# Performance work log

Hardware: AMD Instinct MI355X
Metric: run time of the kernel (lower is better)

## Reference

```python
import jax, jax.numpy as jnp
import numpy as np

DIM = 768
NUM_HEADS = 12
HEAD_DIM = DIM // NUM_HEADS
SCALE = HEAD_DIM ** (-0.5)


def setup_inputs() -> dict:
    key = jax.random.key(0)
    ks = jax.random.split(key, 8)
    B, Nq, Nk, Nv = 2, 2048, 2048, 2048
    init = 0.02
    return {
        "xq": jax.random.normal(ks[0], (B, Nq, DIM), dtype=jnp.float32),
        "xk": jax.random.normal(ks[1], (B, Nk, DIM), dtype=jnp.float32),
        "xv": jax.random.normal(ks[2], (B, Nv, DIM), dtype=jnp.float32),
        # torch nn.Linear weights are [out_features, in_features]; qkv_bias=False
        "Wq": jax.random.normal(ks[3], (DIM, DIM), dtype=jnp.float32) * init,
        "Wk": jax.random.normal(ks[4], (DIM, DIM), dtype=jnp.float32) * init,
        "Wv": jax.random.normal(ks[5], (DIM, DIM), dtype=jnp.float32) * init,
        "Wp": jax.random.normal(ks[6], (DIM, DIM), dtype=jnp.float32) * init,
        "bp": jax.random.normal(ks[7], (DIM,), dtype=jnp.float32) * init,
    }


def reference(xq, xk, xv, Wq, Wk, Wv, Wp, bp):
    B, Nq, C = xq.shape
    H, D = NUM_HEADS, HEAD_DIM
    # linear projections (torch Linear: x @ W.T), split heads -> [B, H, N, D]
    q = (xq @ Wq.T).reshape(B, Nq, H, D).transpose(0, 2, 1, 3)
    k = (xk @ Wk.T).reshape(B, xk.shape[1], H, D).transpose(0, 2, 1, 3)
    v = (xv @ Wv.T).reshape(B, xv.shape[1], H, D).transpose(0, 2, 1, 3)
    # attention scores [B, H, Nq, Nk]
    attn = jnp.einsum("bhqd,bhkd->bhqk", q, k) * SCALE
    attn = jax.nn.softmax(attn, axis=-1)
    # weighted values -> merge heads [B, Nq, C]
    out = jnp.einsum("bhqk,bhkd->bhqd", attn, v)
    out = out.transpose(0, 2, 1, 3).reshape(B, Nq, C)
    return out @ Wp.T + bp
```

## Files before the change

kernel.cpp:

```cpp
#include <hip/hip_runtime.h>
#include <hip/hip_bf16.h>


#define NSEQ 2048
#define CDIM 768
#define NH   12
#define HD   64
#define MTOT 4096
#define XEL  (MTOT*CDIM)
#define WEL  (CDIM*CDIM)
#define X8   (XEL/8)
#define W8   (WEL/8)
#define PSTR 72
#define QSCALE 0.18033688011112042f

typedef __attribute__((ext_vector_type(8))) short bf16x8;
typedef __attribute__((ext_vector_type(4))) float floatx4;

static __device__ __forceinline__ unsigned short f2bf(float f) {
  union { float f; unsigned int u; } v; v.f = f;
  return (unsigned short)((v.u + 0x8000u) >> 16);
}
static __device__ __forceinline__ unsigned pk2bf(float a, float b) {
  unsigned ua = __float_as_uint(a) + 0x8000u;
  unsigned ub = __float_as_uint(b) + 0x8000u;
  return __builtin_amdgcn_perm(ub, ua, 0x07060302);
}

static __device__ __forceinline__ void lds16(const void* g, void* l) {
  __builtin_amdgcn_global_load_lds(
      (const __attribute__((address_space(1))) unsigned int*)g,
      (__attribute__((address_space(3))) unsigned int*)l, 16, 0, 0);
}

__global__ __launch_bounds__(256) void cast_all(
    const float* __restrict__ xq, const float* __restrict__ xk,
    const float* __restrict__ xv, const float* __restrict__ wq,
    const float* __restrict__ wk, const float* __restrict__ wv,
    const float* __restrict__ wp,
    unsigned short* __restrict__ Xq, unsigned short* __restrict__ Xk,
    unsigned short* __restrict__ Xv, unsigned short* __restrict__ Wq,
    unsigned short* __restrict__ Wk, unsigned short* __restrict__ Wv,
    unsigned short* __restrict__ Wp) {
  int i = blockIdx.x * 256 + threadIdx.x;
  const float* s; unsigned short* d; int off;
  if (i < 3 * X8) {
    int t = i / X8; off = i - t * X8;
    s = (t == 0) ? xq : (t == 1) ? xk : xv;
    d = (t == 0) ? Xq : (t == 1) ? Xk : Xv;
  } else {
    int j = i - 3 * X8; int t = j / W8; off = j - t * W8;
    s = (t == 0) ? wq : (t == 1) ? wk : (t == 2) ? wv : wp;
    d = (t == 0) ? Wq : (t == 1) ? Wk : (t == 2) ? Wv : Wp;
  }
  const float4* sp = (const float4*)s + (size_t)off * 2;
  float4 a = sp[0], b = sp[1];
  uint4 o;
  o.x = pk2bf(a.x, a.y); o.y = pk2bf(a.z, a.w);
  o.z = pk2bf(b.x, b.y); o.w = pk2bf(b.z, b.w);
  *(uint4*)(d + (size_t)off * 8) = o;
}

__global__ __launch_bounds__(256) void gemm_qkv(
    const unsigned short* __restrict__ Xq, const unsigned short* __restrict__ Xk,
    const unsigned short* __restrict__ Xv, const unsigned short* __restrict__ Wq,
    const unsigned short* __restrict__ Wk, const unsigned short* __restrict__ Wv,
    unsigned short* __restrict__ Qo, unsigned short* __restrict__ Ko,
    unsigned short* __restrict__ Vo) {
  int i0 = blockIdx.x;
  int mg = i0 & 7; int t0 = i0 >> 3;
  int z = t0 % 3; int u = t0 / 3;
  int xn = u & 7, ysub = u >> 3;
  int y = mg * 4 + ysub;
  const unsigned short* A; const unsigned short* B; int am0, bn0, RA;
  if (z == 0)      { A = Xq; B = Wq; am0 = y * 128; bn0 = xn * 96; RA = 128; }
  else if (z == 1) { A = Xk; B = Wk; am0 = y * 128; bn0 = xn * 96; RA = 128; }
  else             { A = Wv; B = Xv; am0 = xn * 96; bn0 = y * 128; RA = 96; }
  __shared__ __align__(16) unsigned short S[224 * 64];
  int tid = threadIdx.x, lane = tid & 63, wave = tid >> 6;
  int quad = lane >> 4, l15 = lane & 15, l7 = l15 & 7;

  const unsigned short* gptr[7]; int ldo[7];
#pragma unroll
  for (int i = 0; i < 7; i++) {
    int idx = i * 256 + tid;
    int row = idx >> 3, c = (idx & 7) ^ (row & 7);
    gptr[i] = (row < RA ? A + (size_t)(am0 + row) * CDIM
                        : B + (size_t)(bn0 + row - RA) * CDIM) + c * 8;
    ldo[i] = idx * 8;
  }
  floatx4 acc[12];
#pragma unroll
  for (int i = 0; i < 12; i++) acc[i] = (floatx4){0.f, 0.f, 0.f, 0.f};

  for (int k0 = 0; k0 < CDIM; k0 += 64) {
#pragma unroll
    for (int i = 0; i < 7; i++) lds16(gptr[i] + k0, &S[ldo[i]]);
    __syncthreads();
    if (z < 2) {
      int wm = (wave >> 1) * 64, wn = (wave & 1) * 48;
#pragma unroll
      for (int ks = 0; ks < 2; ks++) {
        int csw = ((ks * 4 + quad) ^ l7) * 8;
        bf16x8 af[4], bfr[3];
#pragma unroll
        for (int i = 0; i < 4; i++)
          af[i] = *(const bf16x8*)&S[(wm + i * 16 + l15) * 64 + csw];
#pragma unroll
        for (int j = 0; j < 3; j++)
          bfr[j] = *(const bf16x8*)&S[(128 + wn + j * 16 + l15) * 64 + csw];
#pragma unroll
        for (int mi = 0; mi < 4; mi++)
#pragma unroll
          for (int ni = 0; ni < 3; ni++)
            acc[mi * 3 + ni] = __builtin_amdgcn_mfma_f32_16x16x32_bf16(
                af[mi], bfr[ni], acc[mi * 3 + ni], 0, 0, 0);
      }
    } else {
      int wm = (wave & 1) * 48, wn = (wave >> 1) * 64;
#pragma unroll
      for (int ks = 0; ks < 2; ks++) {
        int csw = ((ks * 4 + quad) ^ l7) * 8;
        bf16x8 af[3], bfr[4];
#pragma unroll
        for (int i = 0; i < 3; i++)
          af[i] = *(const bf16x8*)&S[(wm + i * 16 + l15) * 64 + csw];
#pragma unroll
        for (int j = 0; j < 4; j++)
          bfr[j] = *(const bf16x8*)&S[(96 + wn + j * 16 + l15) * 64 + csw];
#pragma unroll
        for (int mi = 0; mi < 3; mi++)
#pragma unroll
          for (int ni = 0; ni < 4; ni++)
            acc[mi * 4 + ni] = __builtin_amdgcn_mfma_f32_16x16x32_bf16(
                af[mi], bfr[ni], acc[mi * 4 + ni], 0, 0, 0);
      }
    }
    __syncthreads();
  }
  if (z < 2) {
    int wm = (wave >> 1) * 64, wn = (wave & 1) * 48;
#pragma unroll
    for (int mi = 0; mi < 4; mi++)
#pragma unroll
      for (int ni = 0; ni < 3; ni++)
#pragma unroll
        for (int r = 0; r < 4; r++) {
          int grow = am0 + wm + mi * 16 + quad * 4 + r;
          int gcol = bn0 + wn + ni * 16 + l15;
          float v = acc[mi * 3 + ni][r];
          int b = grow >> 11, nq = grow & 2047, h = gcol >> 6, dd = gcol & 63;
          if (z == 0)
            Qo[((size_t)(b * NH + h) * NSEQ + nq) * HD + dd] = f2bf(v * QSCALE);
          else
            Ko[((size_t)(b * NH + h) * NSEQ + nq) * HD + dd] = f2bf(v);
        }
  } else {
    int wm = (wave & 1) * 48, wn = (wave >> 1) * 64;
#pragma unroll
    for (int mi = 0; mi < 3; mi++)
#pragma unroll
      for (int ni = 0; ni < 4; ni++)
#pragma unroll
        for (int r = 0; r < 4; r++) {
          int o = am0 + wm + mi * 16 + quad * 4 + r;
          int mgl = bn0 + wn + ni * 16 + l15;
          int b = mgl >> 11, nq = mgl & 2047;
          Vo[((size_t)b * CDIM + o) * NSEQ + nq] = f2bf(acc[mi * 4 + ni][r]);
        }
  }
}

__global__ __launch_bounds__(256, 3) void attn_kernel(
    const unsigned short* __restrict__ Q, const unsigned short* __restrict__ K,
    const unsigned short* __restrict__ Vt, unsigned short* __restrict__ ctx) {
  int i0 = blockIdx.x;
  int xcd = i0 & 7; int t0 = i0 >> 3;
  int bh = xcd * 3 + (t0 >> 5);
  int qt = t0 & 31;
  int tid = threadIdx.x, lane = tid & 63, wave = tid >> 6;
  int half = wave >> 1, qsub = wave & 1;
  int quad = lane >> 4, l15 = lane & 15, l7 = l15 & 7;
  __shared__ __align__(16) unsigned short Ks[2][64 * 64];
  __shared__ __align__(16) unsigned short Vs[2][64 * 64];
  __shared__ __align__(16) unsigned short Ps[4][16 * PSTR];

  const unsigned short* Qg = Q + ((size_t)bh * NSEQ + qt * 64 + qsub * 32) * HD;
  const unsigned short* Kg = K + ((size_t)bh * NSEQ + half * 1024) * HD;
  const unsigned short* Vg = Vt + (size_t)bh * HD * NSEQ + half * 1024;

  bf16x8 qf[2][2];
#pragma unroll
  for (int qi = 0; qi < 2; qi++)
#pragma unroll
    for (int ks = 0; ks < 2; ks++)
      qf[qi][ks] = *(const bf16x8*)(Qg + (qi * 16 + l15) * HD + ks * 32 + quad * 8);

  bf16x8 ones;
#pragma unroll
  for (int i = 0; i < 8; i++) ones[i] = (short)0x3F80;

  int tid2 = tid & 127;
  int kgo[4], vgo[4], ldst[4];
#pragma unroll
  for (int i = 0; i < 4; i++) {
    int idx = i * 128 + tid2;
    int R = idx >> 3, c = (idx & 7) ^ (R & 7);
    kgo[i] = R * HD + c * 8;
    vgo[i] = R * NSEQ + c * 8;
    ldst[i] = idx * 8;
  }
  unsigned short* Ksh = Ks[half];
  unsigned short* Vsh = Vs[half];
  unsigned short* Pw = &Ps[wave][0];

  floatx4 ol[2];
  floatx4 o[2][4];
#pragma unroll
  for (int qi = 0; qi < 2; qi++) {
    ol[qi] = (floatx4){0.f, 0.f, 0.f, 0.f};
#pragma unroll
    for (int dt = 0; dt < 4; dt++) o[qi][dt] = (floatx4){0.f, 0.f, 0.f, 0.f};
  }

  for (int t = 0; t < 16; t++) {
    int k0 = t * 64;
#pragma unroll
    for (int i = 0; i < 4; i++) {
      lds16(Kg + (size_t)k0 * HD + kgo[i], &Ksh[ldst[i]]);
      lds16(Vg + k0 + vgo[i], &Vsh[ldst[i]]);
    }
    __syncthreads();
    bf16x8 kf[4][2], vf[4][2];
#pragma unroll
    for (int nt = 0; nt < 4; nt++)
#pragma unroll
      for (int x = 0; x < 2; x++)
        kf[nt][x] = *(const bf16x8*)&Ksh[(nt * 16 + l15) * 64 + ((x * 4 + quad) ^ l7) * 8];
#pragma unroll
    for (int dt = 0; dt < 4; dt++)
#pragma unroll
      for (int x = 0; x < 2; x++)
        vf[dt][x] = *(const bf16x8*)&Vsh[(dt * 16 + l15) * 64 + ((x * 4 + quad) ^ l7) * 8];
#pragma unroll
    for (int qi = 0; qi < 2; qi++) {
#pragma unroll
      for (int nt = 0; nt < 4; nt++) {
        floatx4 st = (floatx4){0.f, 0.f, 0.f, 0.f};
        st = __builtin_amdgcn_mfma_f32_16x16x32_bf16(kf[nt][0], qf[qi][0], st, 0, 0, 0);
        st = __builtin_amdgcn_mfma_f32_16x16x32_bf16(kf[nt][1], qf[qi][1], st, 0, 0, 0);
        float p0 = __builtin_exp2f(st[0]), p1 = __builtin_exp2f(st[1]);
        float p2 = __builtin_exp2f(st[2]), p3 = __builtin_exp2f(st[3]);
        *(uint2*)&Pw[l15 * PSTR + nt * 16 + quad * 4] =
            make_uint2(pk2bf(p0, p1), pk2bf(p2, p3));
      }
#pragma unroll
      for (int ks = 0; ks < 2; ks++) {
        bf16x8 pf = *(const bf16x8*)&Pw[l15 * PSTR + ks * 32 + quad * 8];
        ol[qi] = __builtin_amdgcn_mfma_f32_16x16x32_bf16(ones, pf, ol[qi], 0, 0, 0);
#pragma unroll
        for (int dt = 0; dt < 4; dt++)
          o[qi][dt] = __builtin_amdgcn_mfma_f32_16x16x32_bf16(vf[dt][ks], pf, o[qi][dt], 0, 0, 0);
      }
    }
    __syncthreads();
  }
  float* Obuf = (float*)&Ks[0][0];
  float* Lbuf = (float*)&Ps[0][0];
  if (half == 1) {
#pragma unroll
    for (int qi = 0; qi < 2; qi++) {
      int ro = qsub * 32 + qi * 16 + l15;
#pragma unroll
      for (int dt = 0; dt < 4; dt++)
        *(floatx4*)&Obuf[ro * 64 + dt * 16 + quad * 4] = o[qi][dt];
      if (quad == 0) Lbuf[ro] = ol[qi][0];
    }
  }
  __syncthreads();
  if (half == 0) {
    int b = bh / NH, h = bh - b * NH;
#pragma unroll
    for (int qi = 0; qi < 2; qi++) {
      int ro = qsub * 32 + qi * 16 + l15;
      float inv = 1.f / (ol[qi][0] + Lbuf[ro]);
      int qrow = qt * 64 + ro;
      size_t gbase = (size_t)(b * NSEQ + qrow) * CDIM + h * HD + quad * 4;
#pragma unroll
      for (int dt = 0; dt < 4; dt++) {
        floatx4 ob = *(floatx4*)&Obuf[ro * 64 + dt * 16 + quad * 4];
        float v0 = (o[qi][dt][0] + ob[0]) * inv, v1 = (o[qi][dt][1] + ob[1]) * inv;
        float v2 = (o[qi][dt][2] + ob[2]) * inv, v3 = (o[qi][dt][3] + ob[3]) * inv;
        *(uint2*)&ctx[gbase + dt * 16] = make_uint2(pk2bf(v0, v1), pk2bf(v2, v3));
      }
    }
  }
}

__global__ __launch_bounds__(256) void gemm_out(
    const unsigned short* __restrict__ A, const unsigned short* __restrict__ B,
    const float* __restrict__ bias, float* __restrict__ out) {
  int i0 = blockIdx.x;
  int mg = i0 & 7; int t0 = i0 >> 3;
  int n0 = (t0 & 7) * 96;
  int m0 = (mg * 8 + (t0 >> 3)) * 64;
  __shared__ __align__(16) unsigned short S[160 * 128];
  int tid = threadIdx.x, lane = tid & 63, wave = tid >> 6;
  int quad = lane >> 4, l15 = lane & 15, l7 = l15 & 7;
  int wm = (wave >> 1) * 32, wn = (wave & 1) * 48;
  floatx4 acc[6];
#pragma unroll
  for (int i = 0; i < 6; i++) acc[i] = (floatx4){0.f, 0.f, 0.f, 0.f};

  for (int k0 = 0; k0 < CDIM; k0 += 128) {
#pragma unroll
    for (int i = 0; i < 10; i++) {
      int idx = i * 256 + tid;
      int R = idx >> 4, c4 = idx & 15;
      int cs = (c4 & 8) | ((c4 & 7) ^ (R & 7));
      const unsigned short* g = (R < 64)
          ? A + (size_t)(m0 + R) * CDIM : B + (size_t)(n0 + R - 64) * CDIM;
      lds16(g + k0 + cs * 8, &S[idx * 8]);
    }
    __syncthreads();
#pragma unroll
    for (int ks = 0; ks < 4; ks++) {
      int c = ks * 4 + quad;
      int csw = ((c & 8) | ((c & 7) ^ l7)) * 8;
      bf16x8 af[2], bfr[3];
#pragma unroll
      for (int i = 0; i < 2; i++)
        af[i] = *(const bf16x8*)&S[(wm + i * 16 + l15) * 128 + csw];
#pragma unroll
      for (int j = 0; j < 3; j++)
        bfr[j] = *(const bf16x8*)&S[(64 + wn + j * 16 + l15) * 128 + csw];
#pragma unroll
      for (int mi = 0; mi < 2; mi++)
#pragma unroll
        for (int ni = 0; ni < 3; ni++)
          acc[mi * 3 + ni] = __builtin_amdgcn_mfma_f32_16x16x32_bf16(
              af[mi], bfr[ni], acc[mi * 3 + ni], 0, 0, 0);
    }
    __syncthreads();
  }
  float bv[3];
#pragma unroll
  for (int ni = 0; ni < 3; ni++) bv[ni] = bias[n0 + wn + ni * 16 + l15];
#pragma unroll
  for (int mi = 0; mi < 2; mi++)
#pragma unroll
    for (int ni = 0; ni < 3; ni++)
#pragma unroll
      for (int r = 0; r < 4; r++) {
        int grow = m0 + wm + mi * 16 + quad * 4 + r;
        int gcol = n0 + wn + ni * 16 + l15;
        out[(size_t)grow * CDIM + gcol] = acc[mi * 3 + ni][r] + bv[ni];
      }
}

extern "C" void kernel_launch(void* const* d_in, const int* in_sizes, int n_in,
                              void* d_out, int out_size, void* d_ws, size_t ws_size,
                              hipStream_t stream) {
  const float* xq = (const float*)d_in[0];
  const float* xk = (const float*)d_in[1];
  const float* xv = (const float*)d_in[2];
  const float* wq = (const float*)d_in[3];
  const float* wk = (const float*)d_in[4];
  const float* wv = (const float*)d_in[5];
  const float* wp = (const float*)d_in[6];
  const float* bp = (const float*)d_in[7];
  float* out = (float*)d_out;

  char* p = (char*)d_ws;
  unsigned short* Xq = (unsigned short*)p; p += (size_t)XEL * 2;
  unsigned short* Xk = (unsigned short*)p; p += (size_t)XEL * 2;
  unsigned short* Xv = (unsigned short*)p; p += (size_t)XEL * 2;
  unsigned short* Wq = (unsigned short*)p; p += (size_t)WEL * 2;
  unsigned short* Wk = (unsigned short*)p; p += (size_t)WEL * 2;
  unsigned short* Wv = (unsigned short*)p; p += (size_t)WEL * 2;
  unsigned short* Wp = (unsigned short*)p; p += (size_t)WEL * 2;
  unsigned short* Qb = (unsigned short*)p; p += (size_t)XEL * 2;
  unsigned short* Kb = (unsigned short*)p; p += (size_t)XEL * 2;
  unsigned short* Vb = (unsigned short*)p; p += (size_t)XEL * 2;
  unsigned short* Cx = (unsigned short*)p; p += (size_t)XEL * 2;

  cast_all<<<(3 * X8 + 4 * W8) / 256, 256, 0, stream>>>(
      xq, xk, xv, wq, wk, wv, wp, Xq, Xk, Xv, Wq, Wk, Wv, Wp);

  gemm_qkv<<<768, 256, 0, stream>>>(
      Xq, Xk, Xv, Wq, Wk, Wv, Qb, Kb, Vb);

  attn_kernel<<<768, 256, 0, stream>>>(Qb, Kb, Vb, Cx);

  gemm_out<<<512, 256, 0, stream>>>(Cx, Wp, bp, out);
}
```

Baseline: 185.9 us.

## Load K/V fragments directly from global memory instead of staging through LDS

The attention kernel no longer stages K and V tiles into shared memory with direct-to-LDS loads and block-wide barriers. Each lane now reads its MFMA fragments straight from global memory through per-lane pointers, and the key loop is unrolled by two. This removes two __syncthreads per iteration and the LDS round trip. In exchange, the two waves that share a half now each fetch the same K/V tile from global memory, relying on L1/L2 to absorb the duplication. The O/L reduction buffers become dedicated shared arrays rather than aliasing the old K and P buffers.

```diff
diff --git a/kernel.cpp b/kernel.cpp
--- a/kernel.cpp
+++ b/kernel.cpp
@@ -180,10 +180,10 @@
   int qt = t0 & 31;
   int tid = threadIdx.x, lane = tid & 63, wave = tid >> 6;
   int half = wave >> 1, qsub = wave & 1;
-  int quad = lane >> 4, l15 = lane & 15, l7 = l15 & 7;
-  __shared__ __align__(16) unsigned short Ks[2][64 * 64];
-  __shared__ __align__(16) unsigned short Vs[2][64 * 64];
+  int quad = lane >> 4, l15 = lane & 15;
   __shared__ __align__(16) unsigned short Ps[4][16 * PSTR];
+  __shared__ __align__(16) float Obuf[64 * 64];
+  __shared__ float Lbuf[64];
 
   const unsigned short* Qg = Q + ((size_t)bh * NSEQ + qt * 64 + qsub * 32) * HD;
   const unsigned short* Kg = K + ((size_t)bh * NSEQ + half * 1024) * HD;
@@ -200,18 +200,14 @@
 #pragma unroll
   for (int i = 0; i < 8; i++) ones[i] = (short)0x3F80;
 
-  int tid2 = tid & 127;
-  int kgo[4], vgo[4], ldst[4];
+  const unsigned short* kp[4];
+  const unsigned short* vp[4];
 #pragma unroll
   for (int i = 0; i < 4; i++) {
-    int idx = i * 128 + tid2;
-    int R = idx >> 3, c = (idx & 7) ^ (R & 7);
-    kgo[i] = R * HD + c * 8;
-    vgo[i] = R * NSEQ + c * 8;
-    ldst[i] = idx * 8;
-  }
-  unsigned short* Ksh = Ks[half];
-  unsigned short* Vsh = Vs[half];
+    kp[i] = Kg + (size_t)(i * 16 + l15) * HD + quad * 8;
+    vp[i] = Vg + (size_t)(i * 16 + l15) * NSEQ + quad * 8;
+  }
+
   unsigned short* Pw = &Ps[wave][0];
 
   floatx4 ol[2];
@@ -223,25 +219,22 @@
     for (int dt = 0; dt < 4; dt++) o[qi][dt] = (floatx4){0.f, 0.f, 0.f, 0.f};
   }
 
+#pragma unroll 2
   for (int t = 0; t < 16; t++) {
-    int k0 = t * 64;
-#pragma unroll
-    for (int i = 0; i < 4; i++) {
-      lds16(Kg + (size_t)k0 * HD + kgo[i], &Ksh[ldst[i]]);
-      lds16(Vg + k0 + vgo[i], &Vsh[ldst[i]]);
-    }
-    __syncthreads();
     bf16x8 kf[4][2], vf[4][2];
 #pragma unroll
     for (int nt = 0; nt < 4; nt++)
 #pragma unroll
       for (int x = 0; x < 2; x++)
-        kf[nt][x] = *(const bf16x8*)&Ksh[(nt * 16 + l15) * 64 + ((x * 4 + quad) ^ l7) * 8];
+        kf[nt][x] = *(const bf16x8*)(kp[nt] + x * 32);
 #pragma unroll
     for (int dt = 0; dt < 4; dt++)
 #pragma unroll
       for (int x = 0; x < 2; x++)
-        vf[dt][x] = *(const bf16x8*)&Vsh[(dt * 16 + l15) * 64 + ((x * 4 + quad) ^ l7) * 8];
+        vf[dt][x] = *(const bf16x8*)(vp[dt] + x * 32);
+#pragma unroll
+    for (int i = 0; i < 4; i++) { kp[i] += 64 * HD; vp[i] += 64; }
+
 #pragma unroll
     for (int qi = 0; qi < 2; qi++) {
 #pragma unroll
@@ -263,10 +256,7 @@
           o[qi][dt] = __builtin_amdgcn_mfma_f32_16x16x32_bf16(vf[dt][ks], pf, o[qi][dt], 0, 0, 0);
       }
     }
-    __syncthreads();
-  }
-  float* Obuf = (float*)&Ks[0][0];
-  float* Lbuf = (float*)&Ps[0][0];
+  }
   if (half == 1) {
 #pragma unroll
     for (int qi = 0; qi < 2; qi++) {
```

Measured after the change: 231.5 us. +24.5%, slower.

## Double-buffer K/V tiles, widen attention query tile to 128, add MFMA priority

Applied to the files above, without the earlier changes.

The attention kernel now issues the global-to-LDS copy for the next K/V tile before computing on the current one, using two buffers and explicit vmcnt waits with raw barriers. Each block handles 128 query rows instead of 64, so each K/V tile is reused across more queries, and the grid shrinks to 384 blocks. Occupancy is lowered to 2 blocks per CU. MFMA sections are wrapped in setprio, and the cross-half reduction buffer gets an XOR swizzle to reduce LDS bank conflicts. In exchange the kernel uses more registers and LDS, and 384 blocks give fewer waves to hide latency and may leave the grid unevenly spread across CUs.

```diff
diff --git a/kernel.cpp b/kernel.cpp
--- a/kernel.cpp
+++ b/kernel.cpp
@@ -171,27 +171,27 @@
   }
 }
 
-__global__ __launch_bounds__(256, 3) void attn_kernel(
+__global__ __launch_bounds__(256, 2) void attn_kernel(
     const unsigned short* __restrict__ Q, const unsigned short* __restrict__ K,
     const unsigned short* __restrict__ Vt, unsigned short* __restrict__ ctx) {
   int i0 = blockIdx.x;
   int xcd = i0 & 7; int t0 = i0 >> 3;
-  int bh = xcd * 3 + (t0 >> 5);
-  int qt = t0 & 31;
+  int bh = xcd * 3 + (t0 >> 4);
+  int qt = t0 & 15;
   int tid = threadIdx.x, lane = tid & 63, wave = tid >> 6;
   int half = wave >> 1, qsub = wave & 1;
   int quad = lane >> 4, l15 = lane & 15, l7 = l15 & 7;
-  __shared__ __align__(16) unsigned short Ks[2][64 * 64];
-  __shared__ __align__(16) unsigned short Vs[2][64 * 64];
+  __shared__ __align__(16) unsigned short Ks[2][2][64 * 64];
+  __shared__ __align__(16) unsigned short Vs[2][2][64 * 64];
   __shared__ __align__(16) unsigned short Ps[4][16 * PSTR];
 
-  const unsigned short* Qg = Q + ((size_t)bh * NSEQ + qt * 64 + qsub * 32) * HD;
+  const unsigned short* Qg = Q + ((size_t)bh * NSEQ + qt * 128 + qsub * 64) * HD;
   const unsigned short* Kg = K + ((size_t)bh * NSEQ + half * 1024) * HD;
   const unsigned short* Vg = Vt + (size_t)bh * HD * NSEQ + half * 1024;
 
-  bf16x8 qf[2][2];
-#pragma unroll
-  for (int qi = 0; qi < 2; qi++)
+  bf16x8 qf[4][2];
+#pragma unroll
+  for (int qi = 0; qi < 4; qi++)
 #pragma unroll
     for (int ks = 0; ks < 2; ks++)
       qf[qi][ks] = *(const bf16x8*)(Qg + (qi * 16 + l15) * HD + ks * 32 + quad * 8);
@@ -201,36 +201,51 @@
   for (int i = 0; i < 8; i++) ones[i] = (short)0x3F80;
 
   int tid2 = tid & 127;
-  int kgo[4], vgo[4], ldst[4];
+  const unsigned short* kgp[4]; const unsigned short* vgp[4]; int ldst[4];
 #pragma unroll
   for (int i = 0; i < 4; i++) {
     int idx = i * 128 + tid2;
-    int R = idx >> 3, c = (idx & 7) ^ (R & 7);
-    kgo[i] = R * HD + c * 8;
-    vgo[i] = R * NSEQ + c * 8;
+    int row = idx >> 3, c = (idx & 7) ^ (row & 7);
+    kgp[i] = Kg + (size_t)row * HD + c * 8;
+    vgp[i] = Vg + (size_t)row * NSEQ + c * 8;
     ldst[i] = idx * 8;
   }
-  unsigned short* Ksh = Ks[half];
-  unsigned short* Vsh = Vs[half];
+
   unsigned short* Pw = &Ps[wave][0];
 
-  floatx4 ol[2];
-  floatx4 o[2][4];
-#pragma unroll
-  for (int qi = 0; qi < 2; qi++) {
+  floatx4 ol[4];
+  floatx4 o[4][4];
+#pragma unroll
+  for (int qi = 0; qi < 4; qi++) {
     ol[qi] = (floatx4){0.f, 0.f, 0.f, 0.f};
 #pragma unroll
     for (int dt = 0; dt < 4; dt++) o[qi][dt] = (floatx4){0.f, 0.f, 0.f, 0.f};
   }
 
+#pragma unroll
+  for (int i = 0; i < 4; i++) {
+    lds16(kgp[i], &Ks[half][0][ldst[i]]);
+    lds16(vgp[i], &Vs[half][0][ldst[i]]);
+  }
+
+#pragma unroll 2
   for (int t = 0; t < 16; t++) {
-    int k0 = t * 64;
-#pragma unroll
-    for (int i = 0; i < 4; i++) {
-      lds16(Kg + (size_t)k0 * HD + kgo[i], &Ksh[ldst[i]]);
-      lds16(Vg + k0 + vgo[i], &Vsh[ldst[i]]);
-    }
-    __syncthreads();
+    int cur = t & 1;
+    if (t < 15) {
+      int off = (t + 1) * 64;
+#pragma unroll
+      for (int i = 0; i < 4; i++) {
+        lds16(kgp[i] + (size_t)off * HD, &Ks[half][cur ^ 1][ldst[i]]);
+        lds16(vgp[i] + off, &Vs[half][cur ^ 1][ldst[i]]);
+      }
+      asm volatile("s_waitcnt vmcnt(8)" ::: "memory");
+    } else {
+      asm volatile("s_waitcnt vmcnt(0)" ::: "memory");
+    }
+    __builtin_amdgcn_s_barrier();
+
+    const unsigned short* Ksh = &Ks[half][cur][0];
+    const unsigned short* Vsh = &Vs[half][cur][0];
     bf16x8 kf[4][2], vf[4][2];
 #pragma unroll
     for (int nt = 0; nt < 4; nt++)
@@ -242,13 +257,16 @@
 #pragma unroll
       for (int x = 0; x < 2; x++)
         vf[dt][x] = *(const bf16x8*)&Vsh[(dt * 16 + l15) * 64 + ((x * 4 + quad) ^ l7) * 8];
-#pragma unroll
-    for (int qi = 0; qi < 2; qi++) {
+
+#pragma unroll
+    for (int qi = 0; qi < 4; qi++) {
 #pragma unroll
       for (int nt = 0; nt < 4; nt++) {
         floatx4 st = (floatx4){0.f, 0.f, 0.f, 0.f};
+        __builtin_amdgcn_s_setprio(1);
         st = __builtin_amdgcn_mfma_f32_16x16x32_bf16(kf[nt][0], qf[qi][0], st, 0, 0, 0);
         st = __builtin_amdgcn_mfma_f32_16x16x32_bf16(kf[nt][1], qf[qi][1], st, 0, 0, 0);
+        __builtin_amdgcn_s_setprio(0);
         float p0 = __builtin_exp2f(st[0]), p1 = __builtin_exp2f(st[1]);
         float p2 = __builtin_exp2f(st[2]), p3 = __builtin_exp2f(st[3]);
         *(uint2*)&Pw[l15 * PSTR + nt * 16 + quad * 4] =
@@ -257,23 +275,28 @@
 #pragma unroll
       for (int ks = 0; ks < 2; ks++) {
         bf16x8 pf = *(const bf16x8*)&Pw[l15 * PSTR + ks * 32 + quad * 8];
+        __builtin_amdgcn_s_setprio(1);
         ol[qi] = __builtin_amdgcn_mfma_f32_16x16x32_bf16(ones, pf, ol[qi], 0, 0, 0);
 #pragma unroll
         for (int dt = 0; dt < 4; dt++)
           o[qi][dt] = __builtin_amdgcn_mfma_f32_16x16x32_bf16(vf[dt][ks], pf, o[qi][dt], 0, 0, 0);
-      }
-    }
-    __syncthreads();
-  }
-  float* Obuf = (float*)&Ks[0][0];
-  float* Lbuf = (float*)&Ps[0][0];
+        __builtin_amdgcn_s_setprio(0);
+      }
+    }
+    __builtin_amdgcn_s_barrier();
+  }
+
+  float* Obuf = (float*)&Ks[0][0][0];
+  float* Lbuf = (float*)&Vs[0][0][0];
   if (half == 1) {
 #pragma unroll
-    for (int qi = 0; qi < 2; qi++) {
-      int ro = qsub * 32 + qi * 16 + l15;
-#pragma unroll
-      for (int dt = 0; dt < 4; dt++)
-        *(floatx4*)&Obuf[ro * 64 + dt * 16 + quad * 4] = o[qi][dt];
+    for (int qi = 0; qi < 4; qi++) {
+      int ro = qsub * 64 + qi * 16 + l15;
+#pragma unroll
+      for (int dt = 0; dt < 4; dt++) {
+        int ch = (dt * 4 + quad) ^ (ro & 15);
+        *(floatx4*)&Obuf[ro * 64 + ch * 4] = o[qi][dt];
+      }
       if (quad == 0) Lbuf[ro] = ol[qi][0];
     }
   }
@@ -281,14 +304,15 @@
   if (half == 0) {
     int b = bh / NH, h = bh - b * NH;
 #pragma unroll
-    for (int qi = 0; qi < 2; qi++) {
-      int ro = qsub * 32 + qi * 16 + l15;
+    for (int qi = 0; qi < 4; qi++) {
+      int ro = qsub * 64 + qi * 16 + l15;
       float inv = 1.f / (ol[qi][0] + Lbuf[ro]);
-      int qrow = qt * 64 + ro;
+      int qrow = qt * 128 + ro;
       size_t gbase = (size_t)(b * NSEQ + qrow) * CDIM + h * HD + quad * 4;
 #pragma unroll
       for (int dt = 0; dt < 4; dt++) {
-        floatx4 ob = *(floatx4*)&Obuf[ro * 64 + dt * 16 + quad * 4];
+        int ch = (dt * 4 + quad) ^ (ro & 15);
+        floatx4 ob = *(floatx4*)&Obuf[ro * 64 + ch * 4];
         float v0 = (o[qi][dt][0] + ob[0]) * inv, v1 = (o[qi][dt][1] + ob[1]) * inv;
         float v2 = (o[qi][dt][2] + ob[2]) * inv, v3 = (o[qi][dt][3] + ob[3]) * inv;
         *(uint2*)&ctx[gbase + dt * 16] = make_uint2(pk2bf(v0, v1), pk2bf(v2, v3));
@@ -390,7 +414,7 @@
   gemm_qkv<<<768, 256, 0, stream>>>(
       Xq, Xk, Xv, Wq, Wk, Wv, Qb, Kb, Vb);
 
-  attn_kernel<<<768, 256, 0, stream>>>(Qb, Kb, Vb, Cx);
+  attn_kernel<<<384, 256, 0, stream>>>(Qb, Kb, Vb, Cx);
 
   gemm_out<<<512, 256, 0, stream>>>(Cx, Wp, bp, out);
 }
```

Measured after the change: 198.6 us. +6.8%, slower.

## Switch attention to 32x32x16 MFMA with register-resident P via permlane32 swap

Applied to the files above, without the earlier changes.

Rewrites the attention inner loop to use 32x32x16 bf16 MFMA instructions. The probabilities P now stay in registers, rearranged with v_permlane32_swap instead of a round trip through LDS. The row sum is accumulated in VALU adds rather than with an extra MFMA against a ones vector. This removes the per-wave P scratch buffer and its LDS traffic. The cost is higher register pressure from the 16-wide accumulators and reliance on a gfx950-specific instruction.

```diff
diff --git a/kernel.cpp b/kernel.cpp
--- a/kernel.cpp
+++ b/kernel.cpp
@@ -11,11 +11,12 @@
 #define WEL  (CDIM*CDIM)
 #define X8   (XEL/8)
 #define W8   (WEL/8)
-#define PSTR 72
 #define QSCALE 0.18033688011112042f
 
 typedef __attribute__((ext_vector_type(8))) short bf16x8;
 typedef __attribute__((ext_vector_type(4))) float floatx4;
+typedef __attribute__((ext_vector_type(16))) float floatx16;
+typedef __attribute__((ext_vector_type(4))) unsigned int uintx4;
 
 static __device__ __forceinline__ unsigned short f2bf(float f) {
   union { float f; unsigned int u; } v; v.f = f;
@@ -180,25 +181,19 @@
   int qt = t0 & 31;
   int tid = threadIdx.x, lane = tid & 63, wave = tid >> 6;
   int half = wave >> 1, qsub = wave & 1;
-  int quad = lane >> 4, l15 = lane & 15, l7 = l15 & 7;
+  int l31 = lane & 31, hi = lane >> 5;
   __shared__ __align__(16) unsigned short Ks[2][64 * 64];
   __shared__ __align__(16) unsigned short Vs[2][64 * 64];
-  __shared__ __align__(16) unsigned short Ps[4][16 * PSTR];
+  __shared__ float Lbuf[64];
 
   const unsigned short* Qg = Q + ((size_t)bh * NSEQ + qt * 64 + qsub * 32) * HD;
   const unsigned short* Kg = K + ((size_t)bh * NSEQ + half * 1024) * HD;
   const unsigned short* Vg = Vt + (size_t)bh * HD * NSEQ + half * 1024;
 
-  bf16x8 qf[2][2];
-#pragma unroll
-  for (int qi = 0; qi < 2; qi++)
-#pragma unroll
-    for (int ks = 0; ks < 2; ks++)
-      qf[qi][ks] = *(const bf16x8*)(Qg + (qi * 16 + l15) * HD + ks * 32 + quad * 8);
-
-  bf16x8 ones;
-#pragma unroll
-  for (int i = 0; i < 8; i++) ones[i] = (short)0x3F80;
+  bf16x8 qf[4];
+#pragma unroll
+  for (int dc = 0; dc < 4; dc++)
+    qf[dc] = *(const bf16x8*)(Qg + l31 * HD + dc * 16 + hi * 8);
 
   int tid2 = tid & 127;
   int kgo[4], vgo[4], ldst[4];
@@ -212,16 +207,11 @@
   }
   unsigned short* Ksh = Ks[half];
   unsigned short* Vsh = Vs[half];
-  unsigned short* Pw = &Ps[wave][0];
-
-  floatx4 ol[2];
-  floatx4 o[2][4];
-#pragma unroll
-  for (int qi = 0; qi < 2; qi++) {
-    ol[qi] = (floatx4){0.f, 0.f, 0.f, 0.f};
-#pragma unroll
-    for (int dt = 0; dt < 4; dt++) o[qi][dt] = (floatx4){0.f, 0.f, 0.f, 0.f};
-  }
+
+  floatx16 o[2];
+#pragma unroll
+  for (int dt = 0; dt < 2; dt++) o[dt] = (floatx16)(0.f);
+  float l_acc = 0.f;
 
   for (int t = 0; t < 16; t++) {
     int k0 = t * 64;
@@ -231,69 +221,92 @@
       lds16(Vg + k0 + vgo[i], &Vsh[ldst[i]]);
     }
     __syncthreads();
-    bf16x8 kf[4][2], vf[4][2];
-#pragma unroll
-    for (int nt = 0; nt < 4; nt++)
-#pragma unroll
-      for (int x = 0; x < 2; x++)
-        kf[nt][x] = *(const bf16x8*)&Ksh[(nt * 16 + l15) * 64 + ((x * 4 + quad) ^ l7) * 8];
-#pragma unroll
-    for (int dt = 0; dt < 4; dt++)
-#pragma unroll
-      for (int x = 0; x < 2; x++)
-        vf[dt][x] = *(const bf16x8*)&Vsh[(dt * 16 + l15) * 64 + ((x * 4 + quad) ^ l7) * 8];
-#pragma unroll
-    for (int qi = 0; qi < 2; qi++) {
-#pragma unroll
-      for (int nt = 0; nt < 4; nt++) {
-        floatx4 st = (floatx4){0.f, 0.f, 0.f, 0.f};
-        st = __builtin_amdgcn_mfma_f32_16x16x32_bf16(kf[nt][0], qf[qi][0], st, 0, 0, 0);
-        st = __builtin_amdgcn_mfma_f32_16x16x32_bf16(kf[nt][1], qf[qi][1], st, 0, 0, 0);
-        float p0 = __builtin_exp2f(st[0]), p1 = __builtin_exp2f(st[1]);
-        float p2 = __builtin_exp2f(st[2]), p3 = __builtin_exp2f(st[3]);
-        *(uint2*)&Pw[l15 * PSTR + nt * 16 + quad * 4] =
-            make_uint2(pk2bf(p0, p1), pk2bf(p2, p3));
-      }
-#pragma unroll
-      for (int ks = 0; ks < 2; ks++) {
-        bf16x8 pf = *(const bf16x8*)&Pw[l15 * PSTR + ks * 32 + quad * 8];
-        ol[qi] = __builtin_amdgcn_mfma_f32_16x16x32_bf16(ones, pf, ol[qi], 0, 0, 0);
-#pragma unroll
-        for (int dt = 0; dt < 4; dt++)
-          o[qi][dt] = __builtin_amdgcn_mfma_f32_16x16x32_bf16(vf[dt][ks], pf, o[qi][dt], 0, 0, 0);
+
+    bf16x8 kf[2][4];
+#pragma unroll
+    for (int kb = 0; kb < 2; kb++)
+#pragma unroll
+      for (int dc = 0; dc < 4; dc++) {
+        int R = kb * 32 + l31, c = dc * 2 + hi;
+        kf[kb][dc] = *(const bf16x8*)&Ksh[R * 64 + ((c ^ (R & 7)) * 8)];
+      }
+    bf16x8 vf[2][4];
+#pragma unroll
+    for (int dt = 0; dt < 2; dt++)
+#pragma unroll
+      for (int j = 0; j < 4; j++) {
+        int R = dt * 32 + l31, c = j * 2 + hi;
+        vf[dt][j] = *(const bf16x8*)&Vsh[R * 64 + ((c ^ (R & 7)) * 8)];
+      }
+
+#pragma unroll
+    for (int kb = 0; kb < 2; kb++) {
+      floatx16 st = (floatx16)(0.f);
+#pragma unroll
+      for (int dc = 0; dc < 4; dc++)
+        st = __builtin_amdgcn_mfma_f32_32x32x16_bf16(kf[kb][dc], qf[dc], st, 0, 0, 0);
+      float p[16];
+#pragma unroll
+      for (int r = 0; r < 16; r++) p[r] = __builtin_exp2f(st[r]);
+      l_acc += ((p[0] + p[1]) + (p[2] + p[3])) + ((p[4] + p[5]) + (p[6] + p[7])) +
+               (((p[8] + p[9]) + (p[10] + p[11])) + ((p[12] + p[13]) + (p[14] + p[15])));
+      unsigned w[8];
+#pragma unroll
+      for (int i = 0; i < 8; i++) w[i] = pk2bf(p[2 * i], p[2 * i + 1]);
+#pragma unroll
+      for (int kvs = 0; kvs < 2; kvs++) {
+        unsigned a0 = w[kvs * 4 + 0], b0 = w[kvs * 4 + 2];
+        unsigned a1 = w[kvs * 4 + 1], b1 = w[kvs * 4 + 3];
+        asm volatile("v_permlane32_swap_b32 %0, %1" : "+v"(a0), "+v"(b0));
+        asm volatile("v_permlane32_swap_b32 %0, %1" : "+v"(a1), "+v"(b1));
+        uintx4 pw; pw[0] = a0; pw[1] = a1; pw[2] = b0; pw[3] = b1;
+        bf16x8 pb = *(bf16x8*)&pw;
+#pragma unroll
+        for (int dt = 0; dt < 2; dt++)
+          o[dt] = __builtin_amdgcn_mfma_f32_32x32x16_bf16(
+              vf[dt][kb * 2 + kvs], pb, o[dt], 0, 0, 0);
       }
     }
     __syncthreads();
   }
+
+  unsigned lu = __float_as_uint(l_acc), lv = __float_as_uint(l_acc);
+  asm volatile("v_permlane32_swap_b32 %0, %1" : "+v"(lu), "+v"(lv));
+  float lfull = __uint_as_float(lu) + __uint_as_float(lv);
+
   float* Obuf = (float*)&Ks[0][0];
-  float* Lbuf = (float*)&Ps[0][0];
+  int q = qsub * 32 + l31;
   if (half == 1) {
 #pragma unroll
-    for (int qi = 0; qi < 2; qi++) {
-      int ro = qsub * 32 + qi * 16 + l15;
-#pragma unroll
-      for (int dt = 0; dt < 4; dt++)
-        *(floatx4*)&Obuf[ro * 64 + dt * 16 + quad * 4] = o[qi][dt];
-      if (quad == 0) Lbuf[ro] = ol[qi][0];
-    }
+    for (int dt = 0; dt < 2; dt++)
+#pragma unroll
+      for (int rq = 0; rq < 4; rq++) {
+        int ch = (dt * 8 + rq * 2 + hi) ^ (l31 & 15);
+        floatx4 v4 = {o[dt][rq * 4 + 0], o[dt][rq * 4 + 1],
+                      o[dt][rq * 4 + 2], o[dt][rq * 4 + 3]};
+        *(floatx4*)&Obuf[q * 64 + ch * 4] = v4;
+      }
+    if (lane < 32) Lbuf[qsub * 32 + lane] = lfull;
   }
   __syncthreads();
   if (half == 0) {
     int b = bh / NH, h = bh - b * NH;
-#pragma unroll
-    for (int qi = 0; qi < 2; qi++) {
-      int ro = qsub * 32 + qi * 16 + l15;
-      float inv = 1.f / (ol[qi][0] + Lbuf[ro]);
-      int qrow = qt * 64 + ro;
-      size_t gbase = (size_t)(b * NSEQ + qrow) * CDIM + h * HD + quad * 4;
-#pragma unroll
-      for (int dt = 0; dt < 4; dt++) {
-        floatx4 ob = *(floatx4*)&Obuf[ro * 64 + dt * 16 + quad * 4];
-        float v0 = (o[qi][dt][0] + ob[0]) * inv, v1 = (o[qi][dt][1] + ob[1]) * inv;
-        float v2 = (o[qi][dt][2] + ob[2]) * inv, v3 = (o[qi][dt][3] + ob[3]) * inv;
-        *(uint2*)&ctx[gbase + dt * 16] = make_uint2(pk2bf(v0, v1), pk2bf(v2, v3));
-      }
-    }
+    float inv = 1.f / (lfull + Lbuf[q]);
+    int qrow = qt * 64 + q;
+#pragma unroll
+    for (int dt = 0; dt < 2; dt++)
+#pragma unroll
+      for (int rq = 0; rq < 4; rq++) {
+        int ch = (dt * 8 + rq * 2 + hi) ^ (l31 & 15);
+        floatx4 ob = *(floatx4*)&Obuf[q * 64 + ch * 4];
+        float v0 = (o[dt][rq * 4 + 0] + ob[0]) * inv;
+        float v1 = (o[dt][rq * 4 + 1] + ob[1]) * inv;
+        float v2 = (o[dt][rq * 4 + 2] + ob[2]) * inv;
+        float v3 = (o[dt][rq * 4 + 3] + ob[3]) * inv;
+        size_t gbase = (size_t)(b * NSEQ + qrow) * CDIM + h * HD +
+                       dt * 32 + rq * 8 + hi * 4;
+        *(uint2*)&ctx[gbase] = make_uint2(pk2bf(v0, v1), pk2bf(v2, v3));
+      }
   }
 }
 
```

Result: no change. 186.1 us (+0.1%).
